# Performance work log

Hardware: AMD Instinct MI355X
Metric: run time of the kernel (lower is better)

Reference implementation:

```python
import jax, jax.numpy as jnp
import numpy as np
import math

NEG = -1e9
B, TX, TY, ODIM = 32, 512, 2048, 80


def setup_inputs() -> dict:
    key = jax.random.key(0)
    k1, k2 = jax.random.split(key)
    return {
        "x_m": jax.random.normal(k1, (B, TX, ODIM), jnp.float32),
        "x_logs": jnp.zeros((B, TX, ODIM), jnp.float32),  # mean_only=True -> zeros_like(x_m)
        "z": jax.random.normal(k2, (B, ODIM, TY), jnp.float32),
        "x_mask": jnp.ones((B, 1, TX), jnp.float32),
        "z_mask": jnp.ones((B, 1, TY), jnp.float32),
    }


def maximum_path(logp, mask, tx_len, ty_len):
    """Monotonic alignment search (Glow-TTS Viterbi DP).
    logp: [B, Tx, Ty] log-likelihoods; mask: [B, Tx, Ty]; lengths: [B] int32.
    Returns hard alignment path [B, Tx, Ty] in {0,1}.
    """
    B_, Tx, Ty = logp.shape
    xs = jnp.arange(Tx)
    logp = jnp.where(mask > 0, logp, NEG)

    # Forward DP over mel frames y: f[x,y] = logp[x,y] + max(f[x-1,y-1], f[x,y-1])
    def fwd_step(prev, y):
        v_cur = jnp.where(xs[None, :] == y, NEG, prev)              # stay (invalid on diagonal)
        prev_shift = jnp.concatenate(
            [jnp.full((B_, 1), NEG, logp.dtype), prev[:, :-1]], axis=1)
        v_prev = jnp.where(xs[None, :] == 0,
                           jnp.where(y == 0, jnp.zeros((), logp.dtype), jnp.asarray(NEG, logp.dtype)),
                           prev_shift)                               # advance
        f = logp[:, :, y] + jnp.maximum(v_prev, v_cur)
        return f, f

    _, fcols = jax.lax.scan(fwd_step, jnp.full((B_, Tx), NEG, logp.dtype), jnp.arange(Ty))
    # fcols: [Ty, B, Tx]

    # Backtrack from (tx_len-1, ty_len-1) down to y=0.
    def bwd_step(index, y):
        active = y < ty_len                                          # [B] bool
        row = jax.nn.one_hot(index, Tx, dtype=logp.dtype) * active[:, None].astype(logp.dtype)
        fm1 = fcols[jnp.maximum(y - 1, 0)]                           # [B, Tx]
        f_here = jnp.take_along_axis(fm1, index[:, None], axis=1)[:, 0]
        f_left = jnp.take_along_axis(fm1, jnp.maximum(index - 1, 0)[:, None], axis=1)[:, 0]
        move = (index != 0) & ((index == y) | (f_here < f_left))
        new_index = jnp.where(active & move, index - 1, index)
        return new_index, row

    _, rows = jax.lax.scan(bwd_step, tx_len - 1, jnp.arange(Ty - 1, -1, -1))
    path = jnp.flip(rows, axis=0).transpose(1, 2, 0)                 # [B, Tx, Ty]
    return path * mask


def reference(x_m, x_logs, z, x_mask, z_mask):
    # attn_mask: [B, Tx, Ty]
    attn_mask = x_mask[:, 0, :, None] * z_mask[:, 0, None, :]

    # Gaussian log-likelihood of each frame z[:, :, y] under each text token's N(x_m, exp(x_logs))
    x_s_sq_r = jnp.exp(-2.0 * x_logs)                                # [B, Tx, D]
    logp1 = jnp.sum(-0.5 * math.log(2.0 * math.pi) - x_logs, axis=2)[:, :, None]
    logp2 = jnp.einsum('btd,bdy->bty', x_s_sq_r, -0.5 * z * z)
    logp3 = jnp.einsum('btd,bdy->bty', x_m * x_s_sq_r, z)
    logp4 = jnp.sum(-0.5 * x_m * x_m * x_s_sq_r, axis=2)[:, :, None]
    logp = logp1 + logp2 + logp3 + logp4                             # [B, Tx, Ty]

    tx_len = jnp.sum(x_mask[:, 0, :], axis=1).astype(jnp.int32)
    ty_len = jnp.sum(z_mask[:, 0, :], axis=1).astype(jnp.int32)
    attn = jax.lax.stop_gradient(
        maximum_path(jax.lax.stop_gradient(logp), attn_mask, tx_len, ty_len))

    # Expand token stats to frame level with the hard alignment.
    z_m = jnp.einsum('bxy,bxd->bdy', attn, x_m)                      # [B, D, Ty]
    z_logs = jnp.einsum('bxy,bxd->bdy', attn, x_logs)                # [B, D, Ty]
    log_durations_ = jnp.log(1e-8 + jnp.sum(attn, axis=-1))[:, None, :] * x_mask  # [B, 1, Tx]
    return z_m, z_logs, log_durations_, attn
```

## Files before the change

kernel.cpp:

```cpp
#include <hip/hip_runtime.h>
#include <math.h>

#define B_ 32
#define TX_ 512
#define TY_ 2048
#define D_ 80
#define NEG (-1e9f)
#define PF 8

__global__ __launch_bounds__(128) void prep_kernel(
    const float* __restrict__ x_m, const float* __restrict__ x_logs,
    float* __restrict__ A1, float* __restrict__ A2, float* __restrict__ Cc,
    int* __restrict__ flag)
{
    int row = blockIdx.x;
    int t = threadIdx.x;
    __shared__ float red[128];
    float contrib = 0.f;
    bool nz = false;
    if (t < D_) {
        float xl = x_logs[(size_t)row * D_ + t];
        float xm = x_m[(size_t)row * D_ + t];
        nz = (xl != 0.f);
        float a1 = expf(-2.f * xl);
        float a2 = xm * a1;
        A1[(size_t)row * D_ + t] = a1;
        A2[(size_t)row * D_ + t] = a2;
        contrib = -0.91893853320467274178f - xl - 0.5f * xm * xm * a1;
    }
    unsigned long long m = __ballot(nz);
    if ((t & 63) == 0 && m) atomicOr(flag, 1);
    red[t] = contrib;
    __syncthreads();
    if (t < 64) {
        float v = red[t] + red[t + 64];
        #pragma unroll
        for (int off = 32; off >= 1; off >>= 1) v += __shfl_down(v, off);
        if (t == 0) Cc[row] = v;
    }
}

__global__ __launch_bounds__(256) void lens_kernel(const float* __restrict__ x_mask,
    const float* __restrict__ z_mask, int* __restrict__ lens)
{
    int blk = blockIdx.x; int t = threadIdx.x;
    __shared__ float red[256];
    float s = 0.f;
    if (blk < B_) {
        for (int i = t; i < TX_; i += 256) s += x_mask[(size_t)blk * TX_ + i];
    } else {
        int b = blk - B_;
        for (int i = t; i < TY_; i += 256) s += z_mask[(size_t)b * TY_ + i];
    }
    red[t] = s; __syncthreads();
    for (int off = 128; off >= 1; off >>= 1) {
        if (t < off) red[t] += red[t + off];
        __syncthreads();
    }
    if (t == 0) lens[blk] = (int)(red[0] + 0.5f);
}

__global__ __launch_bounds__(256) void szz_kernel(const float* __restrict__ z,
    float* __restrict__ Szz)
{
    int b = blockIdx.y;
    int y4 = blockIdx.x * 256 + threadIdx.x;
    const float4* zp = (const float4*)(z + (size_t)b * D_ * TY_) + y4;
    float4 s = make_float4(0.f, 0.f, 0.f, 0.f);
    #pragma unroll 4
    for (int d = 0; d < D_; ++d) {
        float4 v = zp[(size_t)d * (TY_ / 4)];
        s.x = fmaf(-0.5f * v.x, v.x, s.x);
        s.y = fmaf(-0.5f * v.y, v.y, s.y);
        s.z = fmaf(-0.5f * v.z, v.z, s.z);
        s.w = fmaf(-0.5f * v.w, v.w, s.w);
    }
    ((float4*)(Szz + (size_t)b * TY_))[y4] = s;
}

__global__ __launch_bounds__(256) void gemm_zero(
    const int* __restrict__ flag,
    const float* __restrict__ x_m, const float* __restrict__ Cc,
    const float* __restrict__ Szz, const float* __restrict__ z,
    const float* __restrict__ x_mask, const float* __restrict__ z_mask,
    float* __restrict__ logpT, int y0, int C)
{
    if (*flag != 0) return;
    __shared__ float xs[D_][136];
    __shared__ float zs[D_][64];
    int b = blockIdx.z;
    int x0 = blockIdx.x * 128;
    int cy0 = blockIdx.y * 64;
    int yy0 = y0 + cy0;
    int tid = threadIdx.x;
    for (int i = tid; i < 128 * D_; i += 256) {
        int m = i / D_, d = i - m * D_;
        xs[d][m] = x_m[((size_t)(b * TX_ + x0 + m)) * D_ + d];
    }
    for (int i = tid; i < D_ * 64; i += 256) {
        int d = i >> 6, n = i & 63;
        zs[d][n] = z[((size_t)(b * D_ + d)) * TY_ + yy0 + n];
    }
    __syncthreads();
    int tm = tid & 15, tn = tid >> 4;
    float acc[8][4];
    #pragma unroll
    for (int i = 0; i < 8; ++i)
        #pragma unroll
        for (int j = 0; j < 4; ++j) acc[i][j] = 0.f;
    #pragma unroll 4
    for (int k = 0; k < D_; ++k) {
        float4 a0 = *(const float4*)&xs[k][tm * 8];
        float4 a1v = *(const float4*)&xs[k][tm * 8 + 4];
        float4 zv = *(const float4*)&zs[k][tn * 4];
        float av[8] = {a0.x, a0.y, a0.z, a0.w, a1v.x, a1v.y, a1v.z, a1v.w};
        float zvv[4] = {zv.x, zv.y, zv.z, zv.w};
        #pragma unroll
        for (int j = 0; j < 4; ++j)
            #pragma unroll
            for (int i = 0; i < 8; ++i)
                acc[i][j] = fmaf(av[i], zvv[j], acc[i][j]);
    }
    float4 cc0 = *(const float4*)&Cc[(size_t)b * TX_ + x0 + tm * 8];
    float4 cc1 = *(const float4*)&Cc[(size_t)b * TX_ + x0 + tm * 8 + 4];
    float4 xm0 = *(const float4*)&x_mask[(size_t)b * TX_ + x0 + tm * 8];
    float4 xm1 = *(const float4*)&x_mask[(size_t)b * TX_ + x0 + tm * 8 + 4];
    float ccv[8] = {cc0.x, cc0.y, cc0.z, cc0.w, cc1.x, cc1.y, cc1.z, cc1.w};
    float xmv[8] = {xm0.x, xm0.y, xm0.z, xm0.w, xm1.x, xm1.y, xm1.z, xm1.w};
    #pragma unroll
    for (int j = 0; j < 4; ++j) {
        int n = tn * 4 + j;
        float zmv = z_mask[(size_t)b * TY_ + yy0 + n];
        float sz = Szz[(size_t)b * TY_ + yy0 + n];
        float4 o0, o1;
        float* ov0 = (float*)&o0; float* ov1 = (float*)&o1;
        #pragma unroll
        for (int i = 0; i < 4; ++i) {
            float v0 = acc[i][j] + ccv[i] + sz;
            float v1 = acc[i + 4][j] + ccv[i + 4] + sz;
            ov0[i] = (xmv[i] * zmv > 0.f) ? v0 : NEG;
            ov1[i] = (xmv[i + 4] * zmv > 0.f) ? v1 : NEG;
        }
        float* orow = &logpT[((size_t)b * C + cy0 + n) * TX_ + x0 + tm * 8];
        *(float4*)orow = o0;
        *(float4*)(orow + 4) = o1;
    }
}

__global__ __launch_bounds__(256) void gemm_logp(
    const int* __restrict__ flag,
    const float* __restrict__ A1, const float* __restrict__ A2, const float* __restrict__ Cc,
    const float* __restrict__ z, const float* __restrict__ x_mask, const float* __restrict__ z_mask,
    float* __restrict__ logpT, int y0, int C)
{
    if (*flag == 0) return;
    __shared__ float A1s[D_][72];
    __shared__ float A2s[D_][72];
    __shared__ float zs[D_][64];
    int b = blockIdx.z;
    int x0 = blockIdx.x * 64;
    int cy0 = blockIdx.y * 64;
    int yy0 = y0 + cy0;
    int tid = threadIdx.x;
    for (int i = tid; i < 64 * D_; i += 256) {
        int m = i / D_, d = i - m * D_;
        size_t ga = ((size_t)(b * TX_ + x0 + m)) * D_ + d;
        A1s[d][m] = A1[ga];
        A2s[d][m] = A2[ga];
    }
    for (int i = tid; i < D_ * 64; i += 256) {
        int d = i >> 6, n = i & 63;
        zs[d][n] = z[((size_t)(b * D_ + d)) * TY_ + yy0 + n];
    }
    __syncthreads();
    int tm = tid & 15, tn = tid >> 4;
    float acc[4][4];
    #pragma unroll
    for (int i = 0; i < 4; ++i)
        #pragma unroll
        for (int j = 0; j < 4; ++j) acc[i][j] = 0.f;
    #pragma unroll 4
    for (int k = 0; k < D_; ++k) {
        float4 a1 = *(const float4*)&A1s[k][tm * 4];
        float4 a2 = *(const float4*)&A2s[k][tm * 4];
        float4 zv = *(const float4*)&zs[k][tn * 4];
        float av1[4] = {a1.x, a1.y, a1.z, a1.w};
        float av2[4] = {a2.x, a2.y, a2.z, a2.w};
        float zvv[4] = {zv.x, zv.y, zv.z, zv.w};
        #pragma unroll
        for (int j = 0; j < 4; ++j) {
            float h = -0.5f * zvv[j];
            #pragma unroll
            for (int i = 0; i < 4; ++i) {
                float tt = fmaf(h, av1[i], av2[i]);
                acc[i][j] = fmaf(zvv[j], tt, acc[i][j]);
            }
        }
    }
    float4 cc = *(const float4*)&Cc[(size_t)b * TX_ + x0 + tm * 4];
    float4 xm = *(const float4*)&x_mask[(size_t)b * TX_ + x0 + tm * 4];
    float ccv[4] = {cc.x, cc.y, cc.z, cc.w};
    float xmv[4] = {xm.x, xm.y, xm.z, xm.w};
    #pragma unroll
    for (int j = 0; j < 4; ++j) {
        int n = tn * 4 + j;
        float zmv = z_mask[(size_t)b * TY_ + yy0 + n];
        float4 o;
        float* ov = (float*)&o;
        #pragma unroll
        for (int i = 0; i < 4; ++i) {
            float val = acc[i][j] + ccv[i];
            ov[i] = (xmv[i] * zmv > 0.f) ? val : NEG;
        }
        *(float4*)&logpT[((size_t)b * C + cy0 + n) * TX_ + x0 + tm * 4] = o;
    }
}

__device__ __forceinline__ void dp_stepN(int lane, const float4 la, const float4 lb,
    float (&f)[8], unsigned int laneMask, unsigned char* bpp)
{
    float lp[8] = {la.x, la.y, la.z, la.w, lb.x, lb.y, lb.z, lb.w};
    float sh = __shfl_up(f[7], 1);
    float pm0 = (lane == 0) ? NEG : sh;
    unsigned int byte = 0u;
    #pragma unroll
    for (int j = 7; j >= 0; --j) {
        float pm = (j == 0) ? pm0 : f[j - 1];
        byte = byte * 2u + ((f[j] < pm) ? 1u : 0u);
        f[j] = lp[j] + fmaxf(pm, f[j]);
    }
    *bpp = (unsigned char)(byte & laneMask);
}

__device__ __forceinline__ void dp_stepD(int y, int lane, const float4 la, const float4 lb,
    float (&f)[8], unsigned int laneMask, unsigned char* bpp)
{
    float lp[8] = {la.x, la.y, la.z, la.w, lb.x, lb.y, lb.z, lb.w};
    float sh = __shfl_up(f[7], 1);
    float edge = (y == 0) ? 0.f : NEG;
    float pm0 = (lane == 0) ? edge : sh;
    bool lanehit = (lane == (y >> 3));
    int jeq = y & 7;
    unsigned int byte = 0u;
    #pragma unroll
    for (int j = 7; j >= 0; --j) {
        float pm = (j == 0) ? pm0 : f[j - 1];
        bool ceq = lanehit && (jeq == j);
        byte = byte * 2u + (((f[j] < pm) || ceq) ? 1u : 0u);
        float vc = ceq ? NEG : f[j];
        f[j] = lp[j] + fmaxf(pm, vc);
    }
    *bpp = (unsigned char)(byte & laneMask);
}

__global__ __launch_bounds__(64) void dp_forward(const float* __restrict__ logpT,
    float* __restrict__ fsave, unsigned char* __restrict__ bits8, int y0, int C)
{
    int b = blockIdx.x, lane = threadIdx.x;
    const float* lp = logpT + (size_t)b * C * TX_ + lane * 8;
    unsigned char* bp = bits8 + ((size_t)b * TY_ + y0) * 64 + lane;
    float f[8];
    if (y0 == 0) {
        #pragma unroll
        for (int j = 0; j < 8; ++j) f[j] = NEG;
    } else {
        float4 fa = *(const float4*)(fsave + (size_t)b * TX_ + lane * 8);
        float4 fb = *(const float4*)(fsave + (size_t)b * TX_ + lane * 8 + 4);
        f[0]=fa.x; f[1]=fa.y; f[2]=fa.z; f[3]=fa.w;
        f[4]=fb.x; f[5]=fb.y; f[6]=fb.z; f[7]=fb.w;
    }
    unsigned int laneMask = (lane == 0) ? 0xFEu : 0xFFu;

    float4 bufA[PF], bufB[PF];
    #pragma unroll
    for (int s = 0; s < PF; ++s) {
        int tt = (s < C) ? s : C - 1;
        bufA[s] = *(const float4*)(lp + (size_t)tt * TX_);
        bufB[s] = *(const float4*)(lp + (size_t)tt * TX_ + 4);
    }
    int tD = 0;
    if (y0 < TX_) { tD = TX_ - y0; if (tD > C) tD = C; }
    int t = 0;
    for (; t < tD; t += PF) {
        #pragma unroll
        for (int s = 0; s < PF; ++s) {
            dp_stepD(y0 + t + s, lane, bufA[s], bufB[s], f, laneMask, bp + (size_t)(t + s) * 64);
            int tn = t + s + PF; if (tn >= C) tn = C - 1;
            bufA[s] = *(const float4*)(lp + (size_t)tn * TX_);
            bufB[s] = *(const float4*)(lp + (size_t)tn * TX_ + 4);
        }
    }
    for (; t < C; t += PF) {
        #pragma unroll
        for (int s = 0; s < PF; ++s) {
            dp_stepN(lane, bufA[s], bufB[s], f, laneMask, bp + (size_t)(t + s) * 64);
            int tn = t + s + PF; if (tn >= C) tn = C - 1;
            bufA[s] = *(const float4*)(lp + (size_t)tn * TX_);
            bufB[s] = *(const float4*)(lp + (size_t)tn * TX_ + 4);
        }
    }
    float4 fa = make_float4(f[0], f[1], f[2], f[3]);
    float4 fb = make_float4(f[4], f[5], f[6], f[7]);
    *(float4*)(fsave + (size_t)b * TX_ + lane * 8) = fa;
    *(float4*)(fsave + (size_t)b * TX_ + lane * 8 + 4) = fb;
}

__global__ __launch_bounds__(64) void backtrack_kernel(
    const unsigned char* __restrict__ bits8, const int* __restrict__ lens,
    const float* __restrict__ x_mask, int* __restrict__ idxA, float* __restrict__ logdur)
{
    int b = blockIdx.x, lane = threadIdx.x;
    __shared__ int durS[TX_];
    for (int x = lane; x < TX_; x += 64) durS[x] = 0;
    int tx_len = lens[b];
    int ty_len = lens[B_ + b];
    int idx = tx_len - 1;
    if (idx < 0) idx = 0;
    int cnt = 0;
    const unsigned long long* bu = (const unsigned long long*)(bits8 + (size_t)b * TY_ * 64);
    for (int w = 0; w < TY_ / 64; ++w) {
        int ytop = TY_ - 1 - w * 64;
        int yl = ytop - lane;
        int Whi = idx >> 6;
        unsigned long long whi = bu[(size_t)yl * 8 + Whi];
        unsigned long long wlo = (Whi > 0) ? bu[(size_t)yl * 8 + Whi - 1] : 0ull;
        int rec = -1;
        for (int s = 0; s < 64; ++s) {
            int y = ytop - s;
            bool active = (y < ty_len);
            if (lane == s) rec = active ? idx : -1;
            if (active) cnt++;
            unsigned long long wsel = ((idx >> 6) == Whi) ? __shfl(whi, s) : __shfl(wlo, s);
            int bit = (int)((wsel >> (idx & 63)) & 1ull);
            if (active && bit) {
                if (lane == 0) durS[idx] = cnt;
                cnt = 0;
                idx -= 1;
            }
        }
        idxA[(size_t)b * TY_ + yl] = rec;
    }
    if (lane == 0) durS[idx] = cnt;
    __syncthreads();
    for (int x = lane; x < TX_; x += 64) {
        float dv = (float)durS[x];
        logdur[(size_t)b * TX_ + x] = logf(1e-8f + dv) * x_mask[(size_t)b * TX_ + x];
    }
}

__global__ __launch_bounds__(256) void attn_write(const int* __restrict__ idxA,
    const float* __restrict__ x_mask, const float* __restrict__ z_mask,
    float* __restrict__ attn_o)
{
    int b = blockIdx.z; int x = blockIdx.y;
    int yq = blockIdx.x * 256 + threadIdx.x;
    int4 iv = ((const int4*)(idxA + (size_t)b * TY_))[yq];
    float xm = x_mask[(size_t)b * TX_ + x];
    float4 zm4 = ((const float4*)(z_mask + (size_t)b * TY_))[yq];
    float4 o;
    o.x = (iv.x == x) ? xm * zm4.x : 0.f;
    o.y = (iv.y == x) ? xm * zm4.y : 0.f;
    o.z = (iv.z == x) ? xm * zm4.z : 0.f;
    o.w = (iv.w == x) ? xm * zm4.w : 0.f;
    ((float4*)(attn_o + ((size_t)(b * TX_ + x)) * TY_))[yq] = o;
}

__global__ __launch_bounds__(256) void zm_write(const int* __restrict__ idxA,
    const float* __restrict__ x_m, const float* __restrict__ x_logs,
    const float* __restrict__ x_mask, const float* __restrict__ z_mask,
    float* __restrict__ z_m_o, float* __restrict__ z_logs_o)
{
    int b = blockIdx.z; int d = blockIdx.y;
    int yq = blockIdx.x * 256 + threadIdx.x;
    int4 iv = ((const int4*)(idxA + (size_t)b * TY_))[yq];
    float4 zm4 = ((const float4*)(z_mask + (size_t)b * TY_))[yq];
    float4 om, ol;
    float* omv = (float*)&om; float* olv = (float*)&ol;
    int ivv[4] = {iv.x, iv.y, iv.z, iv.w};
    float zmv[4] = {zm4.x, zm4.y, zm4.z, zm4.w};
    #pragma unroll
    for (int c = 0; c < 4; ++c) {
        float vm = 0.f, vl = 0.f;
        int ix = ivv[c];
        if (ix >= 0) {
            float wgt = x_mask[(size_t)b * TX_ + ix] * zmv[c];
            size_t ga = ((size_t)(b * TX_ + ix)) * D_ + d;
            vm = wgt * x_m[ga];
            vl = wgt * x_logs[ga];
        }
        omv[c] = vm; olv[c] = vl;
    }
    ((float4*)(z_m_o    + ((size_t)(b * D_ + d)) * TY_))[yq] = om;
    ((float4*)(z_logs_o + ((size_t)(b * D_ + d)) * TY_))[yq] = ol;
}

extern "C" void kernel_launch(void* const* d_in, const int* in_sizes, int n_in,
                              void* d_out, int out_size, void* d_ws, size_t ws_size,
                              hipStream_t stream)
{
    const float* x_m    = (const float*)d_in[0];
    const float* x_logs = (const float*)d_in[1];
    const float* z      = (const float*)d_in[2];
    const float* x_mask = (const float*)d_in[3];
    const float* z_mask = (const float*)d_in[4];
    float* out = (float*)d_out;
    float* z_m_o    = out;
    float* z_logs_o = out + (size_t)B_ * D_ * TY_;
    float* logdur_o = out + (size_t)2 * B_ * D_ * TY_;
    float* attn_o   = logdur_o + (size_t)B_ * TX_;

    char* p = (char*)d_ws;
    float* A1 = (float*)p;            p += (size_t)B_ * TX_ * D_ * 4;
    float* A2 = (float*)p;            p += (size_t)B_ * TX_ * D_ * 4;
    float* Cc = (float*)p;            p += (size_t)B_ * TX_ * 4;
    float* fs = (float*)p;            p += (size_t)B_ * TX_ * 4;
    unsigned char* bits8 = (unsigned char*)p; p += (size_t)B_ * TY_ * 64;
    int* idxA = (int*)p;              p += (size_t)B_ * TY_ * 4;
    int* lens = (int*)p;              p += 256;
    int* flag = (int*)p;              p += 256;
    float* Szz = (float*)p;           p += (size_t)B_ * TY_ * 4;
    float* logpC = (float*)p;
    size_t fixed = (size_t)(p - (char*)d_ws);
    size_t avail = (ws_size > fixed) ? (ws_size - fixed) : 0;
    int C = 64;
    const int cands[5] = {2048, 1024, 512, 256, 128};
    for (int i = 0; i < 5; ++i) {
        if ((size_t)B_ * cands[i] * TX_ * 4 <= avail) { C = cands[i]; break; }
    }

    hipMemsetAsync(flag, 0, sizeof(int), stream);
    prep_kernel<<<B_ * TX_, 128, 0, stream>>>(x_m, x_logs, A1, A2, Cc, flag);
    lens_kernel<<<2 * B_, 256, 0, stream>>>(x_mask, z_mask, lens);
    szz_kernel<<<dim3(TY_ / 4 / 256, B_), 256, 0, stream>>>(z, Szz);
    int nc = TY_ / C;
    for (int c = 0; c < nc; ++c) {
        gemm_zero<<<dim3(TX_ / 128, C / 64, B_), 256, 0, stream>>>(
            flag, x_m, Cc, Szz, z, x_mask, z_mask, logpC, c * C, C);
        gemm_logp<<<dim3(TX_ / 64, C / 64, B_), 256, 0, stream>>>(
            flag, A1, A2, Cc, z, x_mask, z_mask, logpC, c * C, C);
        dp_forward<<<B_, 64, 0, stream>>>(logpC, fs, bits8, c * C, C);
    }
    backtrack_kernel<<<B_, 64, 0, stream>>>(bits8, lens, x_mask, idxA, logdur_o);
    attn_write<<<dim3(TY_ / 4 / 256, TX_, B_), 256, 0, stream>>>(idxA, x_mask, z_mask, attn_o);
    zm_write<<<dim3(TY_ / 4 / 256, D_, B_), 256, 0, stream>>>(
        idxA, x_m, x_logs, x_mask, z_mask, z_m_o, z_logs_o);
}
```

Measured before the change: 693.4 us.

## Fuse z-squared sum into GEMM, stage DP backpointer bytes in LDS, deepen prefetch

Measured after the change: 705.9 us. About the same (+1.8%).

```diff
diff --git a/kernel.cpp b/kernel.cpp
--- a/kernel.cpp
+++ b/kernel.cpp
@@ -6,7 +6,7 @@
 #define TY_ 2048
 #define D_ 80
 #define NEG (-1e9f)
-#define PF 8
+#define PF 16
 
 __global__ __launch_bounds__(128) void prep_kernel(
     const float* __restrict__ x_m, const float* __restrict__ x_logs,
@@ -60,28 +60,10 @@
     if (t == 0) lens[blk] = (int)(red[0] + 0.5f);
 }
 
-__global__ __launch_bounds__(256) void szz_kernel(const float* __restrict__ z,
-    float* __restrict__ Szz)
-{
-    int b = blockIdx.y;
-    int y4 = blockIdx.x * 256 + threadIdx.x;
-    const float4* zp = (const float4*)(z + (size_t)b * D_ * TY_) + y4;
-    float4 s = make_float4(0.f, 0.f, 0.f, 0.f);
-    #pragma unroll 4
-    for (int d = 0; d < D_; ++d) {
-        float4 v = zp[(size_t)d * (TY_ / 4)];
-        s.x = fmaf(-0.5f * v.x, v.x, s.x);
-        s.y = fmaf(-0.5f * v.y, v.y, s.y);
-        s.z = fmaf(-0.5f * v.z, v.z, s.z);
-        s.w = fmaf(-0.5f * v.w, v.w, s.w);
-    }
-    ((float4*)(Szz + (size_t)b * TY_))[y4] = s;
-}
-
 __global__ __launch_bounds__(256) void gemm_zero(
     const int* __restrict__ flag,
     const float* __restrict__ x_m, const float* __restrict__ Cc,
-    const float* __restrict__ Szz, const float* __restrict__ z,
+    const float* __restrict__ z,
     const float* __restrict__ x_mask, const float* __restrict__ z_mask,
     float* __restrict__ logpT, int y0, int C)
 {
@@ -104,6 +86,7 @@
     __syncthreads();
     int tm = tid & 15, tn = tid >> 4;
     float acc[8][4];
+    float accz[4] = {0.f, 0.f, 0.f, 0.f};
     #pragma unroll
     for (int i = 0; i < 8; ++i)
         #pragma unroll
@@ -116,10 +99,12 @@
         float av[8] = {a0.x, a0.y, a0.z, a0.w, a1v.x, a1v.y, a1v.z, a1v.w};
         float zvv[4] = {zv.x, zv.y, zv.z, zv.w};
         #pragma unroll
-        for (int j = 0; j < 4; ++j)
+        for (int j = 0; j < 4; ++j) {
+            accz[j] = fmaf(zvv[j], zvv[j], accz[j]);
             #pragma unroll
             for (int i = 0; i < 8; ++i)
                 acc[i][j] = fmaf(av[i], zvv[j], acc[i][j]);
+        }
     }
     float4 cc0 = *(const float4*)&Cc[(size_t)b * TX_ + x0 + tm * 8];
     float4 cc1 = *(const float4*)&Cc[(size_t)b * TX_ + x0 + tm * 8 + 4];
@@ -131,7 +116,7 @@
     for (int j = 0; j < 4; ++j) {
         int n = tn * 4 + j;
         float zmv = z_mask[(size_t)b * TY_ + yy0 + n];
-        float sz = Szz[(size_t)b * TY_ + yy0 + n];
+        float sz = -0.5f * accz[j];
         float4 o0, o1;
         float* ov0 = (float*)&o0; float* ov1 = (float*)&o1;
         #pragma unroll
@@ -216,41 +201,41 @@
     }
 }
 
-__device__ __forceinline__ void dp_stepN(int lane, const float4 la, const float4 lb,
-    float (&f)[8], unsigned int laneMask, unsigned char* bpp)
-{
-    float lp[8] = {la.x, la.y, la.z, la.w, lb.x, lb.y, lb.z, lb.w};
+__device__ __forceinline__ unsigned int dp_stepN_b(int lane, const float4 la, const float4 lb,
+    float (&f)[8], unsigned int laneMask)
+{
+    float lp8[8] = {la.x, la.y, la.z, la.w, lb.x, lb.y, lb.z, lb.w};
     float sh = __shfl_up(f[7], 1);
     float pm0 = (lane == 0) ? NEG : sh;
-    unsigned int byte = 0u;
+    unsigned int byt = 0u;
     #pragma unroll
     for (int j = 7; j >= 0; --j) {
         float pm = (j == 0) ? pm0 : f[j - 1];
-        byte = byte * 2u + ((f[j] < pm) ? 1u : 0u);
-        f[j] = lp[j] + fmaxf(pm, f[j]);
-    }
-    *bpp = (unsigned char)(byte & laneMask);
-}
-
-__device__ __forceinline__ void dp_stepD(int y, int lane, const float4 la, const float4 lb,
-    float (&f)[8], unsigned int laneMask, unsigned char* bpp)
-{
-    float lp[8] = {la.x, la.y, la.z, la.w, lb.x, lb.y, lb.z, lb.w};
+        byt = byt * 2u + ((f[j] < pm) ? 1u : 0u);
+        f[j] = lp8[j] + fmaxf(pm, f[j]);
+    }
+    return byt & laneMask;
+}
+
+__device__ __forceinline__ unsigned int dp_stepD_b(int y, int lane, const float4 la, const float4 lb,
+    float (&f)[8], unsigned int laneMask)
+{
+    float lp8[8] = {la.x, la.y, la.z, la.w, lb.x, lb.y, lb.z, lb.w};
     float sh = __shfl_up(f[7], 1);
     float edge = (y == 0) ? 0.f : NEG;
     float pm0 = (lane == 0) ? edge : sh;
     bool lanehit = (lane == (y >> 3));
     int jeq = y & 7;
-    unsigned int byte = 0u;
+    unsigned int byt = 0u;
     #pragma unroll
     for (int j = 7; j >= 0; --j) {
         float pm = (j == 0) ? pm0 : f[j - 1];
         bool ceq = lanehit && (jeq == j);
-        byte = byte * 2u + (((f[j] < pm) || ceq) ? 1u : 0u);
+        byt = byt * 2u + (((f[j] < pm) || ceq) ? 1u : 0u);
         float vc = ceq ? NEG : f[j];
-        f[j] = lp[j] + fmaxf(pm, vc);
-    }
-    *bpp = (unsigned char)(byte & laneMask);
+        f[j] = lp8[j] + fmaxf(pm, vc);
+    }
+    return byt & laneMask;
 }
 
 __global__ __launch_bounds__(64) void dp_forward(const float* __restrict__ logpT,
@@ -258,7 +243,8 @@
 {
     int b = blockIdx.x, lane = threadIdx.x;
     const float* lp = logpT + (size_t)b * C * TX_ + lane * 8;
-    unsigned char* bp = bits8 + ((size_t)b * TY_ + y0) * 64 + lane;
+    unsigned char* bbase = bits8 + ((size_t)b * TY_ + y0) * 64;
+    __shared__ unsigned char sb[16 * 64];
     float f[8];
     if (y0 == 0) {
         #pragma unroll
@@ -274,30 +260,35 @@
     float4 bufA[PF], bufB[PF];
     #pragma unroll
     for (int s = 0; s < PF; ++s) {
-        int tt = (s < C) ? s : C - 1;
-        bufA[s] = *(const float4*)(lp + (size_t)tt * TX_);
-        bufB[s] = *(const float4*)(lp + (size_t)tt * TX_ + 4);
+        bufA[s] = *(const float4*)(lp + (size_t)s * TX_);
+        bufB[s] = *(const float4*)(lp + (size_t)s * TX_ + 4);
     }
     int tD = 0;
     if (y0 < TX_) { tD = TX_ - y0; if (tD > C) tD = C; }
     int t = 0;
-    for (; t < tD; t += PF) {
-        #pragma unroll
-        for (int s = 0; s < PF; ++s) {
-            dp_stepD(y0 + t + s, lane, bufA[s], bufB[s], f, laneMask, bp + (size_t)(t + s) * 64);
+    for (; t < tD; t += 16) {
+        #pragma unroll
+        for (int s = 0; s < 16; ++s) {
+            unsigned int byt = dp_stepD_b(y0 + t + s, lane, bufA[s], bufB[s], f, laneMask);
+            sb[s * 64 + lane] = (unsigned char)byt;
             int tn = t + s + PF; if (tn >= C) tn = C - 1;
             bufA[s] = *(const float4*)(lp + (size_t)tn * TX_);
             bufB[s] = *(const float4*)(lp + (size_t)tn * TX_ + 4);
         }
-    }
-    for (; t < C; t += PF) {
-        #pragma unroll
-        for (int s = 0; s < PF; ++s) {
-            dp_stepN(lane, bufA[s], bufB[s], f, laneMask, bp + (size_t)(t + s) * 64);
+        int4 v = ((const int4*)sb)[lane];
+        *(int4*)(bbase + (size_t)t * 64 + (size_t)lane * 16) = v;
+    }
+    for (; t < C; t += 16) {
+        #pragma unroll
+        for (int s = 0; s < 16; ++s) {
+            unsigned int byt = dp_stepN_b(lane, bufA[s], bufB[s], f, laneMask);
+            sb[s * 64 + lane] = (unsigned char)byt;
             int tn = t + s + PF; if (tn >= C) tn = C - 1;
             bufA[s] = *(const float4*)(lp + (size_t)tn * TX_);
             bufB[s] = *(const float4*)(lp + (size_t)tn * TX_ + 4);
         }
+        int4 v = ((const int4*)sb)[lane];
+        *(int4*)(bbase + (size_t)t * 64 + (size_t)lane * 16) = v;
     }
     float4 fa = make_float4(f[0], f[1], f[2], f[3]);
     float4 fb = make_float4(f[4], f[5], f[6], f[7]);
@@ -418,7 +409,6 @@
     int* idxA = (int*)p;              p += (size_t)B_ * TY_ * 4;
     int* lens = (int*)p;              p += 256;
     int* flag = (int*)p;              p += 256;
-    float* Szz = (float*)p;           p += (size_t)B_ * TY_ * 4;
     float* logpC = (float*)p;
     size_t fixed = (size_t)(p - (char*)d_ws);
     size_t avail = (ws_size > fixed) ? (ws_size - fixed) : 0;
@@ -431,11 +421,10 @@
     hipMemsetAsync(flag, 0, sizeof(int), stream);
     prep_kernel<<<B_ * TX_, 128, 0, stream>>>(x_m, x_logs, A1, A2, Cc, flag);
     lens_kernel<<<2 * B_, 256, 0, stream>>>(x_mask, z_mask, lens);
-    szz_kernel<<<dim3(TY_ / 4 / 256, B_), 256, 0, stream>>>(z, Szz);
     int nc = TY_ / C;
     for (int c = 0; c < nc; ++c) {
         gemm_zero<<<dim3(TX_ / 128, C / 64, B_), 256, 0, stream>>>(
-            flag, x_m, Cc, Szz, z, x_mask, z_mask, logpC, c * C, C);
+            flag, x_m, Cc, z, x_mask, z_mask, logpC, c * C, C);
         gemm_logp<<<dim3(TX_ / 64, C / 64, B_), 256, 0, stream>>>(
             flag, A1, A2, Cc, z, x_mask, z_mask, logpC, c * C, C);
         dp_forward<<<B_, 64, 0, stream>>>(logpC, fs, bits8, c * C, C);
```
